# Optimization experiments

Measured on AMD Instinct MI355X. Metric: run time of the kernel, lower is better.

The kernel has to match this reference:

```python
import jax, jax.numpy as jnp
import numpy as np

N, E = 32768, 524288
MUL = 32        # multiplicity of 0e and 1o in hidden irreps
N_ATTR = 4      # node attr scalars (species one-hot)
N_RAD = 8       # radial basis size
FC_H = 64       # radial MLP hidden width
AVG_NEIGH = 16.0
INV3 = 1.0 / np.sqrt(3.0)  # w3j(1,1,0) contraction coefficient


def setup_inputs() -> dict:
    key = jax.random.key(0)
    ks = jax.random.split(key, 16)
    p = lambda k, s: jax.random.normal(k, s, dtype=jnp.float32)
    return {
        "node_feats": p(ks[0], (N, MUL + 3 * MUL)),
        "node_attrs": jax.random.uniform(ks[1], (N, N_ATTR), dtype=jnp.float32),
        "edge_feats": p(ks[2], (E, N_RAD)),
        "edge_attrs": p(ks[3], (E, 4)),
        "W1s": p(ks[4], (MUL, MUL)),
        "W1v": p(ks[5], (MUL, MUL)),
        "Wf1": p(ks[6], (N_RAD, FC_H)),
        "Wf2": p(ks[7], (FC_H, FC_H)),
        "Wf3": p(ks[8], (FC_H, 4 * MUL)),
        "W2s": p(ks[9], (2 * MUL, 2 * MUL)),
        "W2v": p(ks[10], (2 * MUL, MUL)),
        "Wsc_s": p(ks[11], (MUL, N_ATTR, 2 * MUL)),
        "Wsc_v": p(ks[12], (MUL, N_ATTR, MUL)),
        "edge_index": jax.random.randint(ks[13], (2, E), 0, N),
    }


def reference(node_feats, node_attrs, edge_feats, edge_attrs,
              W1s, W1v, Wf1, Wf2, Wf3, W2s, W2v, Wsc_s, Wsc_v, edge_index):
    silu = jax.nn.silu
    sender, receiver = edge_index[0], edge_index[1]
    xs0 = node_feats[:, :MUL]                      # [N, MUL]   0e scalars
    xv0 = node_feats[:, MUL:].reshape(-1, MUL, 3)  # [N, MUL, 3] 1o vectors

    # linear_1 (irrep-wise, e3nn fan-in normalization)
    xs = (xs0 @ W1s) / np.sqrt(MUL)
    xv = jnp.einsum('nui,uv->nvi', xv0, W1v) / np.sqrt(MUL)

    # radial MLP -> per-edge tensor-product weights
    h = silu((edge_feats @ Wf1) / np.sqrt(N_RAD))
    h = silu((h @ Wf2) / np.sqrt(FC_H))
    w = (h @ Wf3) / np.sqrt(FC_H)                  # [E, 4*MUL]
    w0, w1, w2, w3 = jnp.split(w, 4, axis=1)       # [E, MUL] each

    sh0 = edge_attrs[:, :1]                        # [E, 1]  l=0
    sh1 = edge_attrs[:, 1:4]                       # [E, 3]  l=1
    xs_e = xs[sender]                              # [E, MUL]
    xv_e = xv[sender]                              # [E, MUL, 3]

    # per-edge 'uvu' tensor product paths (only paths landing in 0e/1o kept)
    m_s0 = w0 * xs_e * sh0                                      # 0e x 0e -> 0e
    m_s1 = w3 * jnp.einsum('eui,ei->eu', xv_e, sh1) * INV3      # 1o x 1o -> 0e
    m_v0 = (w1 * xs_e)[:, :, None] * sh1[:, None, :]            # 0e x 1o -> 1o
    m_v1 = (w2 * sh0)[:, :, None] * xv_e                        # 1o x 0e -> 1o

    msg_s = jnp.concatenate([m_s0, m_s1], axis=1)               # [E, 2*MUL]
    msg_v = jnp.concatenate([m_v0, m_v1], axis=1)               # [E, 2*MUL, 3]

    # scatter-add message passing, normalized by avg num neighbours
    agg_s = jax.ops.segment_sum(msg_s, receiver, num_segments=N) / AVG_NEIGH
    agg_v = jax.ops.segment_sum(msg_v, receiver, num_segments=N) / AVG_NEIGH

    # linear_2 to conv output irreps (2*MUL x 0e + MUL x 1o)
    out_s = (agg_s @ W2s) / np.sqrt(2 * MUL)                    # [N, 2*MUL]
    out_v = jnp.einsum('nui,uv->nvi', agg_v, W2v) / np.sqrt(2 * MUL)

    # self connection: FullyConnectedTensorProduct(x_in, node_attrs)
    norm_sc = 1.0 / np.sqrt(MUL * N_ATTR)
    out_s = out_s + jnp.einsum('nu,na,uaw->nw', xs0, node_attrs, Wsc_s) * norm_sc
    out_v = out_v + jnp.einsum('nui,na,uaw->nwi', xv0, node_attrs, Wsc_v) * norm_sc

    # Gate nonlinearity: act(scalars) ++ act(gates) * gated vectors
    scalars = silu(out_s[:, :MUL])
    gates = silu(out_s[:, MUL:])
    gated = out_v * gates[:, :, None]
    new_feats = jnp.concatenate([scalars, gated.reshape(-1, 3 * MUL)], axis=1)

    # resnet add (irreps_layer_out == interaction_irreps_in)
    return node_feats + new_feats
```

## Files before the change

kernel.cpp:

```cpp
#include <hip/hip_runtime.h>
#include <hip/hip_bf16.h>

#define NN 32768
#define NE 524288

typedef __attribute__((ext_vector_type(8))) short short8v;
typedef __attribute__((ext_vector_type(4))) short short4v;
typedef __attribute__((ext_vector_type(4))) float f32x4;
typedef __attribute__((ext_vector_type(4))) float f32x4v;
typedef __attribute__((ext_vector_type(4))) unsigned u32x4;

__device__ __forceinline__ float silu_f(float x){ return x * (1.0f/(1.0f+__expf(-x))); }
__device__ __forceinline__ float bf2f(unsigned short u){ return __uint_as_float(((unsigned)u)<<16); }
__device__ __forceinline__ unsigned short f2bf(float f){
  __hip_bfloat16 b = __float2bfloat16(f);
  return __builtin_bit_cast(unsigned short, b);
}
__device__ __forceinline__ unsigned pk2(float lo, float hi){
  return (unsigned)f2bf(lo) | ((unsigned)f2bf(hi) << 16);
}

#define S32 0.17677669529663687f
#define S8  0.35355339059327373f
#define S64 0.125f
#define R16 0.0625f
#define NSC 0.08838834764831845f
#define INV3F 0.5773502691896258f

__global__ void k_zero(int* __restrict__ p){
  p[blockIdx.x*256 + threadIdx.x] = 0;
}

__global__ void k_hist(const int* __restrict__ eidx, int* __restrict__ deg){
  int e = blockIdx.x*256 + threadIdx.x;
  int r = eidx[NE + e];
  atomicAdd(&deg[r], 1);
}

__global__ void __launch_bounds__(1024) k_scan(const int* __restrict__ deg,
    int* __restrict__ row_start, int* __restrict__ cursor){
  __shared__ int lds[1024];
  int t = threadIdx.x;
  int4 v[8];
  const int4* dg = reinterpret_cast<const int4*>(deg) + t*8;
  int s = 0;
  #pragma unroll
  for (int j=0;j<8;j++){ v[j] = dg[j]; s += v[j].x+v[j].y+v[j].z+v[j].w; }
  lds[t] = s; __syncthreads();
  for (int off=1; off<1024; off<<=1){
    int q = (t>=off)? lds[t-off] : 0; __syncthreads();
    lds[t] += q; __syncthreads();
  }
  int run = (t==0)?0:lds[t-1];
  int4* rs = reinterpret_cast<int4*>(row_start) + t*8;
  int4* cu = reinterpret_cast<int4*>(cursor) + t*8;
  #pragma unroll
  for (int j=0;j<8;j++){
    int4 o;
    o.x = run; run += v[j].x;
    o.y = run; run += v[j].y;
    o.z = run; run += v[j].z;
    o.w = run; run += v[j].w;
    rs[j] = o; cu[j] = o;
  }
  if (t==1023) row_start[NN] = run;
}

__global__ void k_scatter(const int* __restrict__ eidx, int* __restrict__ cursor,
                          int2* __restrict__ esp){
  int e = blockIdx.x*256 + threadIdx.x;
  int r = eidx[NE + e];
  int s = eidx[e];
  int pos = atomicAdd(&cursor[r], 1);
  esp[pos] = make_int2(e, s);
}

#define XT_ITERS 16
__global__ void __launch_bounds__(256) k_xt(const float* __restrict__ nf,
    const float* __restrict__ W1s, const float* __restrict__ W1v,
    float* __restrict__ xtp2){
  __shared__ float rowbuf[256];
  int t = threadIdx.x;
  int c = t & 127, u = c >> 2, comp = c & 3;
  int node = t >> 7;
  const float* W = (comp==0) ? W1s : W1v;
  float wreg[32];
  #pragma unroll
  for (int k=0;k<32;k++) wreg[k] = W[k*32 + u];
  int soff = node*128 + (comp==0 ? 0 : 32 + (comp-1));
  int stride = (comp==0) ? 1 : 3;
  int base = blockIdx.x * (2*XT_ITERS);
  #pragma unroll 1
  for (int it=0; it<XT_ITERS; it++){
    int n0 = base + it*2;
    __syncthreads();
    rowbuf[t] = nf[(size_t)n0*128 + t];
    __syncthreads();
    float acc = 0.f;
    #pragma unroll
    for (int k=0;k<32;k++) acc += rowbuf[soff + k*stride] * wreg[k];
    xtp2[(size_t)(n0+node)*128 + c] = acc * S32;
  }
}

__global__ void k_wprep(const float* __restrict__ Wf1, const float* __restrict__ Wf2,
                        const float* __restrict__ Wf3,
                        const float* __restrict__ W2s, const float* __restrict__ W2v,
                        const float* __restrict__ Wsc_s, const float* __restrict__ Wsc_v,
                        short* __restrict__ wfrag, short* __restrict__ wfe){
  int f = blockIdx.x;
  int l = threadIdx.x;
  int c = l & 15, g = l >> 4;
  short8v pk;
  if (f < 28){
    #pragma unroll
    for (int j=0;j<8;j++){
      int k = ((j&4) ? 16 : 0) + g*4 + (j&3);
      float val;
      if (f < 4){
        int m = f;
        val = (k < 8) ? Wf1[k*64 + m*16 + c]*S8 : 0.f;
      } else if (f < 12){
        int idx = f-4, m = idx>>1, kk = idx&1;
        val = Wf2[(kk*32+k)*64 + m*16 + c]*S64;
      } else {
        int idx = f-12, m = idx>>1, kk = idx&1;
        val = Wf3[(kk*32+k)*128 + m*16 + c]*S64;
        if (m >= 6) val *= INV3F;
      }
      pk[j] = (short)f2bf(val);
    }
    reinterpret_cast<short8v*>(wfrag)[f*64 + l] = pk;
  } else {
    int fe = f - 28, kb = fe/6, p = fe%6;
    #pragma unroll
    for (int j=0;j<8;j++){
      int k = kb*32 + ((j&4) ? 16 : 0) + g*4 + (j&3);
      float val;
      if (p < 4){
        int col = p*16 + c;
        val = (k < 64) ? W2s[k*64 + col]*S64 : Wsc_s[(k-64)*64 + col]*NSC;
      } else {
        int col = (p-4)*16 + c;
        val = (k < 64) ? W2v[k*32 + col]*S64 : Wsc_v[(k-64)*32 + col]*NSC;
      }
      pk[j] = (short)f2bf(val);
    }
    reinterpret_cast<short8v*>(wfe)[fe*64 + l] = pk;
  }
}

__global__ void __launch_bounds__(256) k_mlp2(const float* __restrict__ ef,
    const float* __restrict__ ea, const int2* __restrict__ esp,
    const short* __restrict__ wfrag, unsigned* __restrict__ wpair,
    float* __restrict__ shp){
  int lane = threadIdx.x & 63;
  int wv = threadIdx.x >> 6;
  int tile = blockIdx.x*4 + wv;
  int e_l = lane & 15, g = lane >> 4;
  const short8v* wf = reinterpret_cast<const short8v*>(wfrag);

  int pos = tile*16 + e_l;
  int e = esp[pos].x;
  if (lane < 16){
    f32x4v av = *reinterpret_cast<const f32x4v*>(ea + (size_t)e*4);
    __builtin_nontemporal_store(av, reinterpret_cast<f32x4v*>(shp + (size_t)pos*4));
  }

  short8v bx = {};
  if (lane < 32){
    const float4 xv = *reinterpret_cast<const float4*>(ef + (size_t)e*8 + g*4);
    bx[0]=(short)f2bf(xv.x); bx[1]=(short)f2bf(xv.y);
    bx[2]=(short)f2bf(xv.z); bx[3]=(short)f2bf(xv.w);
  }
  f32x4 a1[4];
  #pragma unroll
  for (int m=0;m<4;m++){
    f32x4 z = {};
    a1[m] = __builtin_amdgcn_mfma_f32_16x16x32_bf16(wf[m*64+lane], bx, z, 0,0,0);
  }
  short8v b2[2];
  #pragma unroll
  for (int m=0;m<4;m++)
    #pragma unroll
    for (int r=0;r<4;r++)
      b2[m>>1][(m&1)*4 + r] = (short)f2bf(silu_f(a1[m][r]));
  f32x4 a2[4] = {};
  #pragma unroll
  for (int kk=0;kk<2;kk++)
    #pragma unroll
    for (int m=0;m<4;m++)
      a2[m] = __builtin_amdgcn_mfma_f32_16x16x32_bf16(wf[(4+2*m+kk)*64+lane], b2[kk], a2[m], 0,0,0);
  short8v b3[2];
  #pragma unroll
  for (int m=0;m<4;m++)
    #pragma unroll
    for (int r=0;r<4;r++)
      b3[m>>1][(m&1)*4 + r] = (short)f2bf(silu_f(a2[m][r]));
  f32x4 a3[8] = {};
  #pragma unroll
  for (int kk=0;kk<2;kk++)
    #pragma unroll
    for (int m=0;m<8;m++)
      a3[m] = __builtin_amdgcn_mfma_f32_16x16x32_bf16(wf[(12+2*m+kk)*64+lane], b3[kk], a3[m], 0,0,0);
  unsigned* dst = wpair + (size_t)tile*1024 + e_l*64;
  #pragma unroll
  for (int mm=0; mm<2; mm++){
    u32x4 o;
    o.x = pk2(a3[mm][0], a3[mm+2][0]);
    o.y = pk2(a3[mm][1], a3[mm+2][1]);
    o.z = pk2(a3[mm][2], a3[mm+2][2]);
    o.w = pk2(a3[mm][3], a3[mm+2][3]);
    __builtin_nontemporal_store(o, reinterpret_cast<u32x4*>(dst + mm*16 + g*4));
    u32x4 o2;
    o2.x = pk2(a3[6+mm][0], a3[4+mm][0]);
    o2.y = pk2(a3[6+mm][1], a3[4+mm][1]);
    o2.z = pk2(a3[6+mm][2], a3[4+mm][2]);
    o2.w = pk2(a3[6+mm][3], a3[4+mm][3]);
    __builtin_nontemporal_store(o2, reinterpret_cast<u32x4*>(dst + 32 + mm*16 + g*4));
  }
}

#define RV_NODES 4
__global__ void __launch_bounds__(256) k_recv(
    const float* __restrict__ shp, const int* __restrict__ row_start,
    const int2* __restrict__ esp, const unsigned* __restrict__ wpair,
    const float* __restrict__ xtp2, unsigned* __restrict__ agg){
  int wv = threadIdx.x >> 6;
  int lane = threadIdx.x & 63;
  int u = lane & 31;
  bool h1 = lane >= 32;
  bool even = (lane & 1) == 0;
  int nbase = (blockIdx.x*4 + wv) * RV_NODES;

#define EDGE_BODY(WP, SH, Q)                                         \
  {                                                                  \
    float wA = bf2f((unsigned short)((WP) & 0xffffu));               \
    float wB = bf2f((unsigned short)((WP) >> 16));                   \
    float x0 = h1 ? (Q).y : (Q).x;                                   \
    float x1 = h1 ? (Q).z : (Q).x;                                   \
    float x2 = h1 ? (Q).w : (Q).x;                                   \
    float c0 = h1 ? (SH).y : (SH).x;                                 \
    float c1 = h1 ? (SH).z : 0.f;                                    \
    float c2 = h1 ? (SH).w : 0.f;                                    \
    a0 += wA*(x0*c0 + x1*c1 + x2*c2);                                \
    float g0 = wB*(h1 ? (SH).x : (SH).y);                            \
    float g1 = wB*(h1 ? (SH).x : (SH).z);                            \
    float g2 = wB*(h1 ? (SH).x : (SH).w);                            \
    a1 += g0*x0; a2 += g1*x1; a3 += g2*x2;                           \
  }

  #pragma unroll 1
  for (int nn=0; nn<RV_NODES; nn++){
    int n = nbase + nn;
    int lo = row_start[n], hi = row_start[n+1];
    float a0=0.f, a1=0.f, a2=0.f, a3=0.f;
    int nb = (hi - lo) >> 2;
    int2 p0, p1, p2, p3;
    if (nb > 0){
      p0 = esp[lo+0]; p1 = esp[lo+1]; p2 = esp[lo+2]; p3 = esp[lo+3];
    }
    #pragma unroll 1
    for (int b=0; b<nb; b++){
      int idx = lo + b*4;
      int2 n0 = esp[idx+4], n1 = esp[idx+5], n2 = esp[idx+6], n3 = esp[idx+7];
      unsigned wp0 = __builtin_nontemporal_load(&wpair[(size_t)(idx+0)*64 + lane]);
      unsigned wp1 = __builtin_nontemporal_load(&wpair[(size_t)(idx+1)*64 + lane]);
      unsigned wp2 = __builtin_nontemporal_load(&wpair[(size_t)(idx+2)*64 + lane]);
      unsigned wp3 = __builtin_nontemporal_load(&wpair[(size_t)(idx+3)*64 + lane]);
      f32x4v sh0 = __builtin_nontemporal_load(reinterpret_cast<const f32x4v*>(shp + (size_t)(idx+0)*4));
      f32x4v sh1 = __builtin_nontemporal_load(reinterpret_cast<const f32x4v*>(shp + (size_t)(idx+1)*4));
      f32x4v sh2 = __builtin_nontemporal_load(reinterpret_cast<const f32x4v*>(shp + (size_t)(idx+2)*4));
      f32x4v sh3 = __builtin_nontemporal_load(reinterpret_cast<const f32x4v*>(shp + (size_t)(idx+3)*4));
      int b0 = __builtin_amdgcn_readfirstlane(p0.y);
      int b1 = __builtin_amdgcn_readfirstlane(p1.y);
      int b2 = __builtin_amdgcn_readfirstlane(p2.y);
      int b3 = __builtin_amdgcn_readfirstlane(p3.y);
      f32x4v q0 = *reinterpret_cast<const f32x4v*>(xtp2 + (size_t)b0*128 + u*4);
      f32x4v q1 = *reinterpret_cast<const f32x4v*>(xtp2 + (size_t)b1*128 + u*4);
      f32x4v q2 = *reinterpret_cast<const f32x4v*>(xtp2 + (size_t)b2*128 + u*4);
      f32x4v q3 = *reinterpret_cast<const f32x4v*>(xtp2 + (size_t)b3*128 + u*4);
      EDGE_BODY(wp0, sh0, q0);
      EDGE_BODY(wp1, sh1, q1);
      EDGE_BODY(wp2, sh2, q2);
      EDGE_BODY(wp3, sh3, q3);
      p0 = n0; p1 = n1; p2 = n2; p3 = n3;
    }
    #pragma unroll 1
    for (int idx = lo + nb*4; idx < hi; ++idx){
      int2 pp = esp[idx];
      int sb = __builtin_amdgcn_readfirstlane(pp.y);
      unsigned wp = __builtin_nontemporal_load(&wpair[(size_t)idx*64 + lane]);
      f32x4v sh = __builtin_nontemporal_load(reinterpret_cast<const f32x4v*>(shp + (size_t)idx*4));
      f32x4v q = *reinterpret_cast<const f32x4v*>(xtp2 + (size_t)sb*128 + u*4);
      EDGE_BODY(wp, sh, q);
    }
    float r0 = __shfl_xor(a0, 1);
    float r1 = __shfl_xor(a1, 1);
    float r2 = __shfl_xor(a2, 1);
    float r3 = __shfl_xor(a3, 1);
    if (even){
      unsigned* ag = agg + (size_t)n*128 + (lane>>1);
      ag[0]  = pk2(a0*R16, r0*R16);
      ag[32] = pk2(a1*R16, r1*R16);
      ag[64] = pk2(a2*R16, r2*R16);
      ag[96] = pk2(a3*R16, r3*R16);
    }
  }
#undef EDGE_BODY
}

__global__ void __launch_bounds__(256) k_epi(
    const float* __restrict__ nf, const float* __restrict__ na,
    const unsigned short* __restrict__ agg, const short* __restrict__ wfe,
    float* __restrict__ out){
  __shared__ float L[4][16][168];
  int wv = threadIdx.x >> 6, lane = threadIdx.x & 63;
  int tile = blockIdx.x*4 + wv;
  int e = lane & 15, g = lane >> 4;
  int n = tile*16 + e;
  const short8v* WE = reinterpret_cast<const short8v*>(wfe);
  const unsigned short* ag = agg + (size_t)n*256;
  const float* nfr = nf + (size_t)n*128;
  float4 nav = *reinterpret_cast<const float4*>(na + (size_t)n*4);

  f32x4 as0={},as1={},as2={},as3={};
  f32x4 av00={},av01={},av10={},av11={},av20={},av21={};

  #pragma unroll
  for (int kb=0; kb<6; kb++){
    short8v bs, bv0, bv1, bv2;
    if (kb < 2){
      int k0 = kb*32 + g*4;
      #pragma unroll
      for (int i=0;i<4;i++){
        short4v qa = *reinterpret_cast<const short4v*>(ag + i*64 + k0);
        short4v qb = *reinterpret_cast<const short4v*>(ag + i*64 + k0 + 16);
        short8v b;
        b[0]=qa[0]; b[1]=qa[1]; b[2]=qa[2]; b[3]=qa[3];
        b[4]=qb[0]; b[5]=qb[1]; b[6]=qb[2]; b[7]=qb[3];
        if (i==0) bs = b; else if (i==1) bv0 = b; else if (i==2) bv1 = b; else bv2 = b;
      }
    } else {
      int u0 = (kb-2)*8 + g;
      float x0 = nfr[u0], x1 = nfr[u0+4];
      bs[0]=(short)f2bf(x0*nav.x); bs[1]=(short)f2bf(x0*nav.y);
      bs[2]=(short)f2bf(x0*nav.z); bs[3]=(short)f2bf(x0*nav.w);
      bs[4]=(short)f2bf(x1*nav.x); bs[5]=(short)f2bf(x1*nav.y);
      bs[6]=(short)f2bf(x1*nav.z); bs[7]=(short)f2bf(x1*nav.w);
      #pragma unroll
      for (int i=0;i<3;i++){
        float y0 = nfr[32 + u0*3 + i], y1 = nfr[32 + (u0+4)*3 + i];
        short8v b;
        b[0]=(short)f2bf(y0*nav.x); b[1]=(short)f2bf(y0*nav.y);
        b[2]=(short)f2bf(y0*nav.z); b[3]=(short)f2bf(y0*nav.w);
        b[4]=(short)f2bf(y1*nav.x); b[5]=(short)f2bf(y1*nav.y);
        b[6]=(short)f2bf(y1*nav.z); b[7]=(short)f2bf(y1*nav.w);
        if (i==0) bv0 = b; else if (i==1) bv1 = b; else bv2 = b;
      }
    }
    as0 = __builtin_amdgcn_mfma_f32_16x16x32_bf16(WE[(kb*6+0)*64+lane], bs, as0, 0,0,0);
    as1 = __builtin_amdgcn_mfma_f32_16x16x32_bf16(WE[(kb*6+1)*64+lane], bs, as1, 0,0,0);
    as2 = __builtin_amdgcn_mfma_f32_16x16x32_bf16(WE[(kb*6+2)*64+lane], bs, as2, 0,0,0);
    as3 = __builtin_amdgcn_mfma_f32_16x16x32_bf16(WE[(kb*6+3)*64+lane], bs, as3, 0,0,0);
    av00 = __builtin_amdgcn_mfma_f32_16x16x32_bf16(WE[(kb*6+4)*64+lane], bv0, av00, 0,0,0);
    av01 = __builtin_amdgcn_mfma_f32_16x16x32_bf16(WE[(kb*6+5)*64+lane], bv0, av01, 0,0,0);
    av10 = __builtin_amdgcn_mfma_f32_16x16x32_bf16(WE[(kb*6+4)*64+lane], bv1, av10, 0,0,0);
    av11 = __builtin_amdgcn_mfma_f32_16x16x32_bf16(WE[(kb*6+5)*64+lane], bv1, av11, 0,0,0);
    av20 = __builtin_amdgcn_mfma_f32_16x16x32_bf16(WE[(kb*6+4)*64+lane], bv2, av20, 0,0,0);
    av21 = __builtin_amdgcn_mfma_f32_16x16x32_bf16(WE[(kb*6+5)*64+lane], bv2, av21, 0,0,0);
  }

  float (*Lw)[168] = L[wv];
  #pragma unroll
  for (int r=0;r<4;r++){
    Lw[e][ 0 + g*4 + r] = silu_f(as0[r]);
    Lw[e][16 + g*4 + r] = silu_f(as1[r]);
    Lw[e][32 + g*4 + r] = silu_f(as2[r]);
    Lw[e][48 + g*4 + r] = silu_f(as3[r]);
    Lw[e][64 + (     g*4 + r)*3 + 0] = av00[r];
    Lw[e][64 + (16 + g*4 + r)*3 + 0] = av01[r];
    Lw[e][64 + (     g*4 + r)*3 + 1] = av10[r];
    Lw[e][64 + (16 + g*4 + r)*3 + 1] = av11[r];
    Lw[e][64 + (     g*4 + r)*3 + 2] = av20[r];
    Lw[e][64 + (16 + g*4 + r)*3 + 2] = av21[r];
  }
  __syncthreads();

  if (g == 0){
    #pragma unroll
    for (int c=0;c<32;c+=4){
      float4 nv = *reinterpret_cast<const float4*>(nfr + c);
      float4 o;
      o.x = nv.x + Lw[e][c  ];
      o.y = nv.y + Lw[e][c+1];
      o.z = nv.z + Lw[e][c+2];
      o.w = nv.w + Lw[e][c+3];
      *reinterpret_cast<float4*>(out + (size_t)n*128 + c) = o;
    }
  } else {
    int q0 = (g-1)*32;
    #pragma unroll
    for (int q=q0; q<q0+32; q+=4){
      float4 nv = *reinterpret_cast<const float4*>(nfr + 32 + q);
      float4 o;
      o.x = nv.x + Lw[e][64+q+0]*Lw[e][32+(q+0)/3];
      o.y = nv.y + Lw[e][64+q+1]*Lw[e][32+(q+1)/3];
      o.z = nv.z + Lw[e][64+q+2]*Lw[e][32+(q+2)/3];
      o.w = nv.w + Lw[e][64+q+3]*Lw[e][32+(q+3)/3];
      *reinterpret_cast<float4*>(out + (size_t)n*128 + 32 + q) = o;
    }
  }
}

extern "C" void kernel_launch(void* const* d_in, const int* in_sizes, int n_in,
                              void* d_out, int out_size, void* d_ws, size_t ws_size,
                              hipStream_t stream) {
  const float* nf    = (const float*)d_in[0];
  const float* na    = (const float*)d_in[1];
  const float* ef    = (const float*)d_in[2];
  const float* ea    = (const float*)d_in[3];
  const float* W1s   = (const float*)d_in[4];
  const float* W1v   = (const float*)d_in[5];
  const float* Wf1   = (const float*)d_in[6];
  const float* Wf2   = (const float*)d_in[7];
  const float* Wf3   = (const float*)d_in[8];
  const float* W2s   = (const float*)d_in[9];
  const float* W2v   = (const float*)d_in[10];
  const float* Wsc_s = (const float*)d_in[11];
  const float* Wsc_v = (const float*)d_in[12];
  const int*   eidx  = (const int*)d_in[13];
  float* out = (float*)d_out;

  char* ws = (char*)d_ws;
  size_t off = 0;
  auto alloc = [&](size_t bytes)->void*{
    void* p = ws + off; off += (bytes + 255) & ~(size_t)255; return p;
  };
  float*    xtp2      = (float*)alloc((size_t)NN*128*4);
  unsigned* wpair     = (unsigned*)alloc((size_t)NE*64*4);
  unsigned* agg       = (unsigned*)alloc((size_t)NN*256*2);
  float*    shp       = (float*)alloc((size_t)NE*16);
  int*      deg       = (int*)alloc((size_t)NN*4);
  int*      row_start = (int*)alloc((size_t)(NN+16)*4);
  int*      cursor    = (int*)alloc((size_t)NN*4);
  int2*     esp       = (int2*)alloc((size_t)(NE+8)*8);
  short*    wfrag     = (short*)alloc((size_t)28*64*8*2);
  short*    wfe       = (short*)alloc((size_t)36*64*8*2);
  if (off > ws_size) return;

  k_zero   <<<NN/256, 256, 0, stream>>>(deg);
  k_hist   <<<NE/256, 256, 0, stream>>>(eidx, deg);
  k_scan   <<<1, 1024, 0, stream>>>(deg, row_start, cursor);
  k_scatter<<<NE/256, 256, 0, stream>>>(eidx, cursor, esp);
  k_xt     <<<NN/(2*XT_ITERS), 256, 0, stream>>>(nf, W1s, W1v, xtp2);
  k_wprep  <<<64, 64, 0, stream>>>(Wf1, Wf2, Wf3, W2s, W2v, Wsc_s, Wsc_v, wfrag, wfe);
  k_mlp2   <<<8192, 256, 0, stream>>>(ef, ea, esp, wfrag, wpair, shp);
  k_recv   <<<NN/(4*RV_NODES), 256, 0, stream>>>(shp, row_start, esp, wpair, xtp2,
                                      (unsigned*)agg);
  k_epi    <<<512, 256, 0, stream>>>(nf, na, (const unsigned short*)agg, wfe, out);
}
```

Before: 255.3 us.

## Pad CSR rows to multiples of four and interleave edge weights per group

Each receiver's edge segment is padded to a multiple of four, and padded slots are marked with -1. The MLP kernel now transposes its output through LDS so that one 16-byte load in the receive kernel fetches the weights for four edges. The receive loop drops its remainder loop, loads the four sender indices with a single int4, and gathers two senders per wave split across the half-waves using shuffles. In exchange there are extra padded edges running through the MLP, extra fill kernels, and LDS traffic in the MLP kernel.

New measurement: 256.6 us. No clear change (+0.5%).

```diff
diff --git a/kernel.cpp b/kernel.cpp
--- a/kernel.cpp
+++ b/kernel.cpp
@@ -3,6 +3,8 @@
 
 #define NN 32768
 #define NE 524288
+#define PADCAP4 (NE + 4*NN)
+#define MLP_TILES (PADCAP4/16)
 
 typedef __attribute__((ext_vector_type(8))) short short8v;
 typedef __attribute__((ext_vector_type(4))) short short4v;
@@ -30,6 +32,9 @@
 __global__ void k_zero(int* __restrict__ p){
   p[blockIdx.x*256 + threadIdx.x] = 0;
 }
+__global__ void k_fillm1(int* __restrict__ p){
+  p[blockIdx.x*256 + threadIdx.x] = -1;
+}
 
 __global__ void k_hist(const int* __restrict__ eidx, int* __restrict__ deg){
   int e = blockIdx.x*256 + threadIdx.x;
@@ -38,21 +43,26 @@
 }
 
 __global__ void __launch_bounds__(1024) k_scan(const int* __restrict__ deg,
-    int* __restrict__ row_start, int* __restrict__ cursor){
+    int* __restrict__ rs_pad, int* __restrict__ cursor){
   __shared__ int lds[1024];
   int t = threadIdx.x;
   int4 v[8];
   const int4* dg = reinterpret_cast<const int4*>(deg) + t*8;
   int s = 0;
   #pragma unroll
-  for (int j=0;j<8;j++){ v[j] = dg[j]; s += v[j].x+v[j].y+v[j].z+v[j].w; }
+  for (int j=0;j<8;j++){
+    v[j] = dg[j];
+    v[j].x = (v[j].x+3)&~3; v[j].y = (v[j].y+3)&~3;
+    v[j].z = (v[j].z+3)&~3; v[j].w = (v[j].w+3)&~3;
+    s += v[j].x+v[j].y+v[j].z+v[j].w;
+  }
   lds[t] = s; __syncthreads();
   for (int off=1; off<1024; off<<=1){
     int q = (t>=off)? lds[t-off] : 0; __syncthreads();
     lds[t] += q; __syncthreads();
   }
   int run = (t==0)?0:lds[t-1];
-  int4* rs = reinterpret_cast<int4*>(row_start) + t*8;
+  int4* rs = reinterpret_cast<int4*>(rs_pad) + t*8;
   int4* cu = reinterpret_cast<int4*>(cursor) + t*8;
   #pragma unroll
   for (int j=0;j<8;j++){
@@ -63,16 +73,17 @@
     o.w = run; run += v[j].w;
     rs[j] = o; cu[j] = o;
   }
-  if (t==1023) row_start[NN] = run;
+  if (t==1023) rs_pad[NN] = run;
 }
 
 __global__ void k_scatter(const int* __restrict__ eidx, int* __restrict__ cursor,
-                          int2* __restrict__ esp){
+                          int* __restrict__ eperm, int* __restrict__ sperm){
   int e = blockIdx.x*256 + threadIdx.x;
   int r = eidx[NE + e];
   int s = eidx[e];
   int pos = atomicAdd(&cursor[r], 1);
-  esp[pos] = make_int2(e, s);
+  eperm[pos] = e;
+  sperm[pos] = s;
 }
 
 #define XT_ITERS 16
@@ -151,25 +162,29 @@
 }
 
 __global__ void __launch_bounds__(256) k_mlp2(const float* __restrict__ ef,
-    const float* __restrict__ ea, const int2* __restrict__ esp,
-    const short* __restrict__ wfrag, unsigned* __restrict__ wpair,
-    float* __restrict__ shp){
+    const float* __restrict__ ea, const int* __restrict__ rs_pad,
+    const int* __restrict__ eperm, const short* __restrict__ wfrag,
+    unsigned* __restrict__ G, float* __restrict__ shp){
+  __shared__ unsigned sb[4][16][68];
   int lane = threadIdx.x & 63;
   int wv = threadIdx.x >> 6;
   int tile = blockIdx.x*4 + wv;
+  if (tile*16 >= rs_pad[NN]) return;
   int e_l = lane & 15, g = lane >> 4;
   const short8v* wf = reinterpret_cast<const short8v*>(wfrag);
 
   int pos = tile*16 + e_l;
-  int e = esp[pos].x;
+  int e = eperm[pos];
+  int ec = e < 0 ? 0 : e;
   if (lane < 16){
-    f32x4v av = *reinterpret_cast<const f32x4v*>(ea + (size_t)e*4);
+    f32x4v av = {0.f,0.f,0.f,0.f};
+    if (e >= 0) av = *reinterpret_cast<const f32x4v*>(ea + (size_t)ec*4);
     __builtin_nontemporal_store(av, reinterpret_cast<f32x4v*>(shp + (size_t)pos*4));
   }
 
   short8v bx = {};
   if (lane < 32){
-    const float4 xv = *reinterpret_cast<const float4*>(ef + (size_t)e*8 + g*4);
+    const float4 xv = *reinterpret_cast<const float4*>(ef + (size_t)ec*8 + g*4);
     bx[0]=(short)f2bf(xv.x); bx[1]=(short)f2bf(xv.y);
     bx[2]=(short)f2bf(xv.z); bx[3]=(short)f2bf(xv.w);
   }
@@ -203,7 +218,6 @@
     #pragma unroll
     for (int m=0;m<8;m++)
       a3[m] = __builtin_amdgcn_mfma_f32_16x16x32_bf16(wf[(12+2*m+kk)*64+lane], b3[kk], a3[m], 0,0,0);
-  unsigned* dst = wpair + (size_t)tile*1024 + e_l*64;
   #pragma unroll
   for (int mm=0; mm<2; mm++){
     u32x4 o;
@@ -211,20 +225,31 @@
     o.y = pk2(a3[mm][1], a3[mm+2][1]);
     o.z = pk2(a3[mm][2], a3[mm+2][2]);
     o.w = pk2(a3[mm][3], a3[mm+2][3]);
-    __builtin_nontemporal_store(o, reinterpret_cast<u32x4*>(dst + mm*16 + g*4));
+    *reinterpret_cast<u32x4*>(&sb[wv][e_l][mm*16 + g*4]) = o;
     u32x4 o2;
     o2.x = pk2(a3[6+mm][0], a3[4+mm][0]);
     o2.y = pk2(a3[6+mm][1], a3[4+mm][1]);
     o2.z = pk2(a3[6+mm][2], a3[4+mm][2]);
     o2.w = pk2(a3[6+mm][3], a3[4+mm][3]);
-    __builtin_nontemporal_store(o2, reinterpret_cast<u32x4*>(dst + 32 + mm*16 + g*4));
+    *reinterpret_cast<u32x4*>(&sb[wv][e_l][32 + mm*16 + g*4]) = o2;
+  }
+  const unsigned* Wd = &sb[wv][0][0];
+  #pragma unroll
+  for (int k=0;k<4;k++){
+    u32x4 o;
+    o.x = Wd[(4*k+0)*68 + lane];
+    o.y = Wd[(4*k+1)*68 + lane];
+    o.z = Wd[(4*k+2)*68 + lane];
+    o.w = Wd[(4*k+3)*68 + lane];
+    __builtin_nontemporal_store(o,
+        reinterpret_cast<u32x4*>(G + ((size_t)(tile*4 + k)*64 + lane)*4));
   }
 }
 
 #define RV_NODES 4
 __global__ void __launch_bounds__(256) k_recv(
-    const float* __restrict__ shp, const int* __restrict__ row_start,
-    const int2* __restrict__ esp, const unsigned* __restrict__ wpair,
+    const float* __restrict__ shp, const int* __restrict__ rs_pad,
+    const int* __restrict__ sperm, const unsigned* __restrict__ G,
     const float* __restrict__ xtp2, unsigned* __restrict__ agg){
   int wv = threadIdx.x >> 6;
   int lane = threadIdx.x & 63;
@@ -253,47 +278,47 @@
   #pragma unroll 1
   for (int nn=0; nn<RV_NODES; nn++){
     int n = nbase + nn;
-    int lo = row_start[n], hi = row_start[n+1];
+    int lo = rs_pad[n], hi = rs_pad[n+1];
     float a0=0.f, a1=0.f, a2=0.f, a3=0.f;
-    int nb = (hi - lo) >> 2;
-    int2 p0, p1, p2, p3;
-    if (nb > 0){
-      p0 = esp[lo+0]; p1 = esp[lo+1]; p2 = esp[lo+2]; p3 = esp[lo+3];
-    }
     #pragma unroll 1
-    for (int b=0; b<nb; b++){
-      int idx = lo + b*4;
-      int2 n0 = esp[idx+4], n1 = esp[idx+5], n2 = esp[idx+6], n3 = esp[idx+7];
-      unsigned wp0 = __builtin_nontemporal_load(&wpair[(size_t)(idx+0)*64 + lane]);
-      unsigned wp1 = __builtin_nontemporal_load(&wpair[(size_t)(idx+1)*64 + lane]);
-      unsigned wp2 = __builtin_nontemporal_load(&wpair[(size_t)(idx+2)*64 + lane]);
-      unsigned wp3 = __builtin_nontemporal_load(&wpair[(size_t)(idx+3)*64 + lane]);
-      f32x4v sh0 = __builtin_nontemporal_load(reinterpret_cast<const f32x4v*>(shp + (size_t)(idx+0)*4));
-      f32x4v sh1 = __builtin_nontemporal_load(reinterpret_cast<const f32x4v*>(shp + (size_t)(idx+1)*4));
-      f32x4v sh2 = __builtin_nontemporal_load(reinterpret_cast<const f32x4v*>(shp + (size_t)(idx+2)*4));
-      f32x4v sh3 = __builtin_nontemporal_load(reinterpret_cast<const f32x4v*>(shp + (size_t)(idx+3)*4));
-      int b0 = __builtin_amdgcn_readfirstlane(p0.y);
-      int b1 = __builtin_amdgcn_readfirstlane(p1.y);
-      int b2 = __builtin_amdgcn_readfirstlane(p2.y);
-      int b3 = __builtin_amdgcn_readfirstlane(p3.y);
-      f32x4v q0 = *reinterpret_cast<const f32x4v*>(xtp2 + (size_t)b0*128 + u*4);
-      f32x4v q1 = *reinterpret_cast<const f32x4v*>(xtp2 + (size_t)b1*128 + u*4);
-      f32x4v q2 = *reinterpret_cast<const f32x4v*>(xtp2 + (size_t)b2*128 + u*4);
-      f32x4v q3 = *reinterpret_cast<const f32x4v*>(xtp2 + (size_t)b3*128 + u*4);
-      EDGE_BODY(wp0, sh0, q0);
-      EDGE_BODY(wp1, sh1, q1);
-      EDGE_BODY(wp2, sh2, q2);
-      EDGE_BODY(wp3, sh3, q3);
-      p0 = n0; p1 = n1; p2 = n2; p3 = n3;
-    }
-    #pragma unroll 1
-    for (int idx = lo + nb*4; idx < hi; ++idx){
-      int2 pp = esp[idx];
-      int sb = __builtin_amdgcn_readfirstlane(pp.y);
-      unsigned wp = __builtin_nontemporal_load(&wpair[(size_t)idx*64 + lane]);
-      f32x4v sh = __builtin_nontemporal_load(reinterpret_cast<const f32x4v*>(shp + (size_t)idx*4));
-      f32x4v q = *reinterpret_cast<const f32x4v*>(xtp2 + (size_t)sb*128 + u*4);
-      EDGE_BODY(wp, sh, q);
+    for (int pos = lo; pos < hi; pos += 4){
+      u32x4 wq = __builtin_nontemporal_load(
+          reinterpret_cast<const u32x4*>(G + ((size_t)(pos>>2)*64 + lane)*4));
+      int4 sv = *reinterpret_cast<const int4*>(sperm + pos);
+      f32x4v sh0 = __builtin_nontemporal_load(reinterpret_cast<const f32x4v*>(shp + (size_t)(pos+0)*4));
+      f32x4v sh1 = __builtin_nontemporal_load(reinterpret_cast<const f32x4v*>(shp + (size_t)(pos+1)*4));
+      f32x4v sh2 = __builtin_nontemporal_load(reinterpret_cast<const f32x4v*>(shp + (size_t)(pos+2)*4));
+      f32x4v sh3 = __builtin_nontemporal_load(reinterpret_cast<const f32x4v*>(shp + (size_t)(pos+3)*4));
+      int b0 = __builtin_amdgcn_readfirstlane(sv.x);
+      int b1 = __builtin_amdgcn_readfirstlane(sv.y);
+      int b2 = __builtin_amdgcn_readfirstlane(sv.z);
+      int b3 = __builtin_amdgcn_readfirstlane(sv.w);
+      {
+        int base = h1 ? b1 : b0;
+        f32x4v q = *reinterpret_cast<const f32x4v*>(xtp2 + (size_t)base*128 + u*4);
+        f32x4v qo;
+        qo.x = __shfl_xor(q.x, 32);
+        qo.y = __shfl_xor(q.y, 32);
+        qo.z = __shfl_xor(q.z, 32);
+        qo.w = __shfl_xor(q.w, 32);
+        f32x4v qA = h1 ? qo : q;
+        f32x4v qB = h1 ? q : qo;
+        EDGE_BODY(wq.x, sh0, qA);
+        EDGE_BODY(wq.y, sh1, qB);
+      }
+      {
+        int base = h1 ? b3 : b2;
+        f32x4v q = *reinterpret_cast<const f32x4v*>(xtp2 + (size_t)base*128 + u*4);
+        f32x4v qo;
+        qo.x = __shfl_xor(q.x, 32);
+        qo.y = __shfl_xor(q.y, 32);
+        qo.z = __shfl_xor(q.z, 32);
+        qo.w = __shfl_xor(q.w, 32);
+        f32x4v qA = h1 ? qo : q;
+        f32x4v qB = h1 ? q : qo;
+        EDGE_BODY(wq.z, sh2, qA);
+        EDGE_BODY(wq.w, sh3, qB);
+      }
     }
     float r0 = __shfl_xor(a0, 1);
     float r1 = __shfl_xor(a1, 1);
@@ -438,25 +463,28 @@
     void* p = ws + off; off += (bytes + 255) & ~(size_t)255; return p;
   };
   float*    xtp2      = (float*)alloc((size_t)NN*128*4);
-  unsigned* wpair     = (unsigned*)alloc((size_t)NE*64*4);
+  unsigned* G         = (unsigned*)alloc((size_t)(PADCAP4/4)*64*16);
   unsigned* agg       = (unsigned*)alloc((size_t)NN*256*2);
-  float*    shp       = (float*)alloc((size_t)NE*16);
+  float*    shp       = (float*)alloc((size_t)PADCAP4*16);
   int*      deg       = (int*)alloc((size_t)NN*4);
-  int*      row_start = (int*)alloc((size_t)(NN+16)*4);
+  int*      rs_pad    = (int*)alloc((size_t)(NN+16)*4);
   int*      cursor    = (int*)alloc((size_t)NN*4);
-  int2*     esp       = (int2*)alloc((size_t)(NE+8)*8);
+  int*      eperm     = (int*)alloc((size_t)PADCAP4*4);
+  int*      sperm     = (int*)alloc((size_t)PADCAP4*4);
   short*    wfrag     = (short*)alloc((size_t)28*64*8*2);
   short*    wfe       = (short*)alloc((size_t)36*64*8*2);
   if (off > ws_size) return;
 
   k_zero   <<<NN/256, 256, 0, stream>>>(deg);
+  k_fillm1 <<<PADCAP4/256, 256, 0, stream>>>(eperm);
+  k_zero   <<<PADCAP4/256, 256, 0, stream>>>(sperm);
   k_hist   <<<NE/256, 256, 0, stream>>>(eidx, deg);
-  k_scan   <<<1, 1024, 0, stream>>>(deg, row_start, cursor);
-  k_scatter<<<NE/256, 256, 0, stream>>>(eidx, cursor, esp);
+  k_scan   <<<1, 1024, 0, stream>>>(deg, rs_pad, cursor);
+  k_scatter<<<NE/256, 256, 0, stream>>>(eidx, cursor, eperm, sperm);
   k_xt     <<<NN/(2*XT_ITERS), 256, 0, stream>>>(nf, W1s, W1v, xtp2);
   k_wprep  <<<64, 64, 0, stream>>>(Wf1, Wf2, Wf3, W2s, W2v, Wsc_s, Wsc_v, wfrag, wfe);
-  k_mlp2   <<<8192, 256, 0, stream>>>(ef, ea, esp, wfrag, wpair, shp);
-  k_recv   <<<NN/(4*RV_NODES), 256, 0, stream>>>(shp, row_start, esp, wpair, xtp2,
-                                      (unsigned*)agg);
+  k_mlp2   <<<MLP_TILES/4, 256, 0, stream>>>(ef, ea, rs_pad, eperm, wfrag, G, shp);
+  k_recv   <<<NN/(4*RV_NODES), 256, 0, stream>>>(shp, rs_pad, sperm, G, xtp2,
+                                                 (unsigned*)agg);
   k_epi    <<<512, 256, 0, stream>>>(nf, na, (const unsigned short*)agg, wfe, out);
 }
```
